# Kernel optimization log

Measured on AMD Instinct MI355X. Metric: run time of the kernel, lower is better.

## Reference

```python
import jax, jax.numpy as jnp
import numpy as np

E = 64      # embedding_dim
H = 64      # h_dim
MLP = 1024  # mlp_dim (attention hidden)
PRE1 = 512  # mlp_pre_pool hidden
BNK = 1024  # bottleneck_dim
S = 256     # num scenes (equal-size groups replacing seq_start_end)
P = 16      # pedestrians per scene
B = S * P   # total batch of pedestrians
T = 8       # obs_len for vx/vy (only last row used)
EPS = 1e-5  # BatchNorm eps


def _bn(x, g, b, m, v):
    # eval-mode BatchNorm1d over the last (feature) axis
    return (x - m) * jax.lax.rsqrt(v + EPS) * g + b


def setup_inputs() -> dict:
    key = jax.random.key(0)
    ks = jax.random.split(key, 24)
    def n(k, shape, s=1.0):
        return jax.random.normal(k, shape, jnp.float32) * s
    return {
        "h_states": n(ks[0], (1, B, H)),
        "end_pos": n(ks[1], (B, 2)),
        "vx": n(ks[2], (T, B)),
        "vy": n(ks[3], (T, B)),
        "W_sp": n(ks[4], (2, E), 0.05), "b_sp": jnp.zeros((E,), jnp.float32),
        "W_vel": n(ks[5], (2, E), 0.05), "b_vel": jnp.zeros((E,), jnp.float32),
        "Wa1": n(ks[6], (2 * E, MLP), 0.05), "ba1": jnp.zeros((MLP,), jnp.float32),
        "ga1": jnp.ones((MLP,), jnp.float32), "bta1": jnp.zeros((MLP,), jnp.float32),
        "ma1": n(ks[7], (MLP,), 0.1), "va1": jax.random.uniform(ks[8], (MLP,), jnp.float32) + 0.5,
        "Wa2": n(ks[9], (MLP, 1), 0.05), "ba2": jnp.zeros((1,), jnp.float32),
        "ga2": jnp.ones((1,), jnp.float32), "bta2": jnp.zeros((1,), jnp.float32),
        "ma2": n(ks[10], (1,), 0.1), "va2": jax.random.uniform(ks[11], (1,), jnp.float32) + 0.5,
        "Wp1": n(ks[12], (E + H, PRE1), 0.05), "bp1": jnp.zeros((PRE1,), jnp.float32),
        "gp1": jnp.ones((PRE1,), jnp.float32), "btp1": jnp.zeros((PRE1,), jnp.float32),
        "mp1": n(ks[13], (PRE1,), 0.1), "vp1": jax.random.uniform(ks[14], (PRE1,), jnp.float32) + 0.5,
        "Wp2": n(ks[15], (PRE1, BNK), 0.05), "bp2": jnp.zeros((BNK,), jnp.float32),
        "gp2": jnp.ones((BNK,), jnp.float32), "btp2": jnp.zeros((BNK,), jnp.float32),
        "mp2": n(ks[16], (BNK,), 0.1), "vp2": jax.random.uniform(ks[17], (BNK,), jnp.float32) + 0.5,
        "num_scenes": S, "num_ped": P,
    }


def _forward(h_states, end_pos, vx, vy, W_sp, b_sp, W_vel, b_vel,
             Wa1, ba1, ga1, bta1, ma1, va1, Wa2, ba2, ga2, bta2, ma2, va2,
             Wp1, bp1, gp1, btp1, mp1, vp1, Wp2, bp2, gp2, btp2, mp2, vp2,
             num_scenes, num_ped):
    Sn, Pn = num_scenes, num_ped
    h = h_states.reshape(-1, H).reshape(Sn, Pn, H)          # per-scene hidden
    pos = end_pos.reshape(Sn, Pn, 2)
    # rel[s,i,j] = pos[s,j] - pos[s,i]  (repeat vs repeat_interleave in torch)
    rel = pos[:, None, :, :] - pos[:, :, None, :]
    rel_emb = rel @ W_sp + b_sp                              # [S,P,P,E]
    vel = jnp.stack([vx[-1], vy[-1]], axis=-1).reshape(Sn, Pn, 2)
    vel_emb = vel @ W_vel + b_vel                            # [S,P,E], indexed by row i
    vel_emb = jnp.broadcast_to(vel_emb[:, :, None, :], (Sn, Pn, Pn, E))
    att_in = jnp.concatenate([rel_emb, vel_emb], axis=-1)    # [S,P,P,2E]
    a = jax.nn.relu(_bn(att_in @ Wa1 + ba1, ga1, bta1, ma1, va1))
    scores = jax.nn.relu(_bn(a @ Wa2 + ba2, ga2, bta2, ma2, va2))  # [S,P,P,1]
    # torch.softmax(scores, dim=1) on an (N,1) tensor: softmax over the size-1
    # feature axis -> identically 1.0. Reproduced faithfully here.
    w = jax.nn.softmax(scores, axis=-1)
    h_rep = jnp.broadcast_to(h[:, None, :, :], (Sn, Pn, Pn, H))   # h[s,j] per (i,j)
    x = jnp.concatenate([rel_emb, h_rep], axis=-1) * (0.05 * w)   # [S,P,P,E+H]
    y = jax.nn.relu(_bn(x @ Wp1 + bp1, gp1, btp1, mp1, vp1))
    y = jax.nn.relu(_bn(y @ Wp2 + bp2, gp2, btp2, mp2, vp2))      # [S,P,P,BNK]
    pool = jnp.max(y, axis=2)                                     # max over neighbors j
    return pool.reshape(Sn * Pn, BNK)


def reference(h_states, end_pos, vx, vy, W_sp, b_sp, W_vel, b_vel,
              Wa1, ba1, ga1, bta1, ma1, va1, Wa2, ba2, ga2, bta2, ma2, va2,
              Wp1, bp1, gp1, btp1, mp1, vp1, Wp2, bp2, gp2, btp2, mp2, vp2,
              num_scenes, num_ped):
    return _forward(h_states, end_pos, vx, vy, W_sp, b_sp, W_vel, b_vel,
                    Wa1, ba1, ga1, bta1, ma1, va1, Wa2, ba2, ga2, bta2, ma2, va2,
                    Wp1, bp1, gp1, btp1, mp1, vp1, Wp2, bp2, gp2, btp2, mp2, vp2,
                    num_scenes, num_ped)
```

## Files before the change

### kernel.cpp

```cpp
#include <hip/hip_runtime.h>
#include <hip/hip_bf16.h>
#include <stdint.h>


typedef __bf16 bf16x8 __attribute__((ext_vector_type(8)));
typedef __bf16 bf16x2 __attribute__((ext_vector_type(2)));
typedef float  f32x4  __attribute__((ext_vector_type(4)));
typedef float  f32x2  __attribute__((ext_vector_type(2)));

#define BP2_OFF 0u
#define BP1_OFF 1048576u
#define MX_OFF  1114112u
#define MY_OFF  1116160u
#define CB_OFF  1118208u
#define SH_OFF  1120256u
#define A2_OFF  1122304u
#define C2_OFF  1126400u

#define Y1_LDS  0
#define HH_LDS  131072
#define LDS_SZ  147456

__device__ __forceinline__ unsigned short f2bf(float f) {
    union { float f; unsigned u; } c; c.f = f;
    unsigned u = c.u;
    return (unsigned short)((u + 0x7fffu + ((u >> 16) & 1u)) >> 16);
}
__device__ __forceinline__ float bfbits2f(unsigned hi) {
    union { unsigned u; float f; } c; c.u = hi; return c.f;
}
__device__ __forceinline__ unsigned pk_bf16(float a, float b) {
#if __has_builtin(__builtin_amdgcn_cvt_pk_bf16_f32)
    bf16x2 p = __builtin_amdgcn_cvt_pk_bf16_f32(a, b);
    union { bf16x2 v; unsigned u; } c; c.v = p; return c.u;
#else
    return (unsigned)f2bf(a) | ((unsigned)f2bf(b) << 16);
#endif
}
__device__ __forceinline__ int y1off(int r, int c16) {
    return r * 1024 + ((c16 ^ (r & 7)) << 4);
}

__global__ __launch_bounds__(256) void prep_pack_kernel(
    const float* __restrict__ Wsp,  const float* __restrict__ bsp,
    const float* __restrict__ Wp1,  const float* __restrict__ bp1,
    const float* __restrict__ gp1,  const float* __restrict__ btp1,
    const float* __restrict__ mp1,  const float* __restrict__ vp1,
    const float* __restrict__ Wp2,  const float* __restrict__ bp2,
    const float* __restrict__ gp2,  const float* __restrict__ btp2,
    const float* __restrict__ mp2,  const float* __restrict__ vp2,
    unsigned char* __restrict__ ws)
{
    __shared__ float tile[32 * 65];
    const int blk = blockIdx.x, t = threadIdx.x;

    if (blk < 272) {
        const float* src; int ncols, kb, ng;
        if (blk < 256) { kb = blk >> 4; ng = blk & 15; src = Wp2; ncols = 1024; }
        else { int b2 = blk - 256; kb = b2 >> 3; ng = b2 & 7; src = Wp1 + 64 * 512; ncols = 512; }
        const int k0 = kb * 32, n0 = ng * 64;
        #pragma unroll
        for (int it = 0; it < 2; ++it) {
            int c = t + it * 256;
            int r = c >> 4, c4 = c & 15;
            float4 v = *(const float4*)(src + (k0 + r) * ncols + n0 + c4 * 4);
            tile[r * 65 + c4 * 4 + 0] = v.x;
            tile[r * 65 + c4 * 4 + 1] = v.y;
            tile[r * 65 + c4 * 4 + 2] = v.z;
            tile[r * 65 + c4 * 4 + 3] = v.w;
        }
        __syncthreads();
        int ntl = t >> 6, l = t & 63;
        int nl = ntl * 16 + (l & 15), kl = (l >> 4) * 8;
        uint4 o;
        o.x = pk_bf16(tile[(kl + 0) * 65 + nl], tile[(kl + 1) * 65 + nl]);
        o.y = pk_bf16(tile[(kl + 2) * 65 + nl], tile[(kl + 3) * 65 + nl]);
        o.z = pk_bf16(tile[(kl + 4) * 65 + nl], tile[(kl + 5) * 65 + nl]);
        o.w = pk_bf16(tile[(kl + 6) * 65 + nl], tile[(kl + 7) * 65 + nl]);
        if (blk < 256) {
            ((uint4*)(ws + BP2_OFF))[(kb * 64 + ng * 4 + ntl) * 64 + l] = o;
        } else {
            ((uint4*)(ws + BP1_OFF))[((ng * 4 + ntl) * 2 + kb) * 64 + l] = o;
        }
    } else if (blk < 274) {
        int k = (blk - 272) * 256 + t;
        float a1 = gp1[k] * rsqrtf(vp1[k] + 1e-5f);
        float mx = 0.f, my = 0.f, cb = 0.f;
        for (int e = 0; e < 64; ++e) {
            float wv = Wp1[e * 512 + k];
            mx = fmaf(Wsp[e],      wv, mx);
            my = fmaf(Wsp[64 + e], wv, my);
            cb = fmaf(bsp[e],      wv, cb);
        }
        ((float*)(ws + MX_OFF))[k] = 0.05f * a1 * mx;
        ((float*)(ws + MY_OFF))[k] = 0.05f * a1 * my;
        ((float*)(ws + CB_OFF))[k] = 0.05f * a1 * cb + (bp1[k] - mp1[k]) * a1 + btp1[k];
        ((float*)(ws + SH_OFF))[k] = 0.05f * a1;
    } else {
        int n = (blk - 274) * 256 + t;
        float a = gp2[n] * rsqrtf(vp2[n] + 1e-5f);
        ((float*)(ws + A2_OFF))[n] = a;
        ((float*)(ws + C2_OFF))[n] = btp2[n] + (bp2[n] - mp2[n]) * a;
    }
}

__global__ __launch_bounds__(512, 2) void mm2_kernel(
    const float* __restrict__ hst,
    const float* __restrict__ epos,
    const unsigned char* __restrict__ ws,
    float* __restrict__ out)
{
    __shared__ __align__(16) unsigned char smem[LDS_SZ];

    const int s   = blockIdx.x >> 1;
    const int ih  = blockIdx.x & 1;
    const int tid = threadIdx.x;
    const int w    = tid >> 6;
    const int l    = tid & 63;
    const int quad = l >> 4;
    const int jl   = l & 15;

    {
        union { unsigned u[4]; bf16x8 v; } afh[2];
        #pragma unroll
        for (int kb = 0; kb < 2; ++kb) {
            const float4* hp = (const float4*)(hst + (s * 16 + jl) * 64 + kb * 32 + quad * 8);
            float4 v0 = hp[0], v1 = hp[1];
            afh[kb].u[0] = pk_bf16(v0.x, v0.y);
            afh[kb].u[1] = pk_bf16(v0.z, v0.w);
            afh[kb].u[2] = pk_bf16(v1.x, v1.y);
            afh[kb].u[3] = pk_bf16(v1.z, v1.w);
        }
        const f32x4 fz = {0.f, 0.f, 0.f, 0.f};
        f32x4 acch[4] = {fz, fz, fz, fz};
        #pragma unroll
        for (int kb = 0; kb < 2; ++kb) {
            #pragma unroll
            for (int ct = 0; ct < 4; ++ct) {
                bf16x8 bfr = *(const bf16x8*)(ws + BP1_OFF + ((((w * 4 + ct) * 2 + kb) * 64 + l) << 4));
                acch[ct] = __builtin_amdgcn_mfma_f32_16x16x32_bf16(afh[kb].v, bfr, acch[ct], 0, 0, 0);
            }
        }
        const float* SHg = (const float*)(ws + SH_OFF);
        const float* CBg = (const float*)(ws + CB_OFF);
        #pragma unroll
        for (int ct = 0; ct < 4; ++ct) {
            int col = (w * 4 + ct) * 16 + jl;
            float sh = SHg[col], cb = CBg[col];
            #pragma unroll
            for (int reg = 0; reg < 4; ++reg) {
                int j = quad * 4 + reg;
                float hv = fmaf(acch[ct][reg], sh, cb);
                *(unsigned short*)(smem + HH_LDS + j * 1024 + col * 2) = f2bf(hv);
            }
        }
    }
    __syncthreads();

    {
        const int i2 = tid >> 8;
        const int j  = (tid >> 4) & 15;
        const int kc = tid & 15;
        float rx[4], ry[4];
        float pjx = epos[s * 32 + j * 2], pjy = epos[s * 32 + j * 2 + 1];
        #pragma unroll
        for (int ii = 0; ii < 4; ++ii) {
            int ig_ = ih * 8 + i2 * 4 + ii;
            rx[ii] = pjx - epos[s * 32 + ig_ * 2];
            ry[ii] = pjy - epos[s * 32 + ig_ * 2 + 1];
        }
        const f32x2 zero2 = {0.f, 0.f};
        #pragma unroll
        for (int kk = 0; kk < 4; ++kk) {
            int k = kc * 32 + kk * 8;
            uint4 hh8 = *(const uint4*)(smem + HH_LDS + j * 1024 + k * 2);
            f32x4 mx0 = *(const f32x4*)(ws + MX_OFF + k * 4);
            f32x4 mx1 = *(const f32x4*)(ws + MX_OFF + k * 4 + 16);
            f32x4 my0 = *(const f32x4*)(ws + MY_OFF + k * 4);
            f32x4 my1 = *(const f32x4*)(ws + MY_OFF + k * 4 + 16);
            f32x2 mxp[4] = { {mx0[0],mx0[1]}, {mx0[2],mx0[3]}, {mx1[0],mx1[1]}, {mx1[2],mx1[3]} };
            f32x2 myp[4] = { {my0[0],my0[1]}, {my0[2],my0[3]}, {my1[0],my1[1]}, {my1[2],my1[3]} };
            f32x2 hhp[4];
            hhp[0][0] = bfbits2f(hh8.x << 16); hhp[0][1] = bfbits2f(hh8.x & 0xffff0000u);
            hhp[1][0] = bfbits2f(hh8.y << 16); hhp[1][1] = bfbits2f(hh8.y & 0xffff0000u);
            hhp[2][0] = bfbits2f(hh8.z << 16); hhp[2][1] = bfbits2f(hh8.z & 0xffff0000u);
            hhp[3][0] = bfbits2f(hh8.w << 16); hhp[3][1] = bfbits2f(hh8.w & 0xffff0000u);
            #pragma unroll
            for (int ii = 0; ii < 4; ++ii) {
                f32x2 rx2 = { rx[ii], rx[ii] };
                f32x2 ry2 = { ry[ii], ry[ii] };
                uint4 o;
                unsigned uu[4];
                #pragma unroll
                for (int p = 0; p < 4; ++p) {
                    f32x2 tt = __builtin_elementwise_fma(ry2, myp[p], hhp[p]);
                    tt = __builtin_elementwise_fma(rx2, mxp[p], tt);
                    tt = __builtin_elementwise_max(tt, zero2);
                    uu[p] = pk_bf16(tt[0], tt[1]);
                }
                o.x = uu[0]; o.y = uu[1]; o.z = uu[2]; o.w = uu[3];
                int r = (i2 * 4 + ii) * 16 + j;
                *(uint4*)(smem + Y1_LDS + y1off(r, kc * 4 + kk)) = o;
            }
        }
    }
    __syncthreads();

    const int ig = w & 1;
    const int ng = w >> 1;
    const float* A2 = (const float*)(ws + A2_OFF);
    const float* C2 = (const float*)(ws + C2_OFF);
    const f32x4 fzero = {0.f, 0.f, 0.f, 0.f};

    int ab[4];
    #pragma unroll
    for (int rt = 0; rt < 4; ++rt) {
        int r = (ig * 4 + rt) * 16 + jl;
        ab[rt] = Y1_LDS + r * 1024 + ((quad ^ (r & 7)) << 4);
    }

    #pragma unroll 1
    for (int chunk = 0; chunk < 2; ++chunk) {
        const int ntbase = ng * 16 + chunk * 8;
        const unsigned char* bp0 = ws + BP2_OFF + (ntbase << 10) + (l << 4);

        f32x4 acc[4][8];
        #pragma unroll
        for (int rt = 0; rt < 4; ++rt)
            #pragma unroll
            for (int ct = 0; ct < 8; ++ct) acc[rt][ct] = fzero;

        bf16x8 b0[8], b1[8];
        #pragma unroll
        for (int ct = 0; ct < 8; ++ct)
            b0[ct] = *(const bf16x8*)(bp0 + ct * 1024);

        #pragma unroll 1
        for (int t = 0; t < 8; ++t) {
            bf16x8 ae[4], ao[4];
            #pragma unroll
            for (int rt = 0; rt < 4; ++rt)
                ae[rt] = *(const bf16x8*)(smem + (ab[rt] + t * 128));
            #pragma unroll
            for (int ct = 0; ct < 8; ++ct)
                b1[ct] = *(const bf16x8*)(bp0 + (2 * t + 1) * 65536 + ct * 1024);
            #pragma unroll
            for (int rt = 0; rt < 4; ++rt)
                ao[rt] = *(const bf16x8*)(smem + ((ab[rt] + t * 128) ^ 64));
            #pragma unroll
            for (int rt = 0; rt < 4; ++rt)
                #pragma unroll
                for (int ct = 0; ct < 8; ++ct)
                    acc[rt][ct] = __builtin_amdgcn_mfma_f32_16x16x32_bf16(ae[rt], b0[ct], acc[rt][ct], 0, 0, 0);
            #pragma unroll
            for (int ct = 0; ct < 8; ++ct)
                b0[ct] = *(const bf16x8*)(bp0 + (2 * t + 2) * 65536 + ct * 1024);
            #pragma unroll
            for (int rt = 0; rt < 4; ++rt)
                #pragma unroll
                for (int ct = 0; ct < 8; ++ct)
                    acc[rt][ct] = __builtin_amdgcn_mfma_f32_16x16x32_bf16(ao[rt], b1[ct], acc[rt][ct], 0, 0, 0);
        }

        #pragma unroll
        for (int ct = 0; ct < 8; ++ct) {
            int col = (ntbase + ct) * 16 + jl;
            float a2 = A2[col], c2 = C2[col];
            #pragma unroll
            for (int rt = 0; rt < 4; ++rt) {
                float v0 = fmaxf(fmaf(acc[rt][ct][0], a2, c2), 0.f);
                float v1 = fmaxf(fmaf(acc[rt][ct][1], a2, c2), 0.f);
                float v2 = fmaxf(fmaf(acc[rt][ct][2], a2, c2), 0.f);
                float v3 = fmaxf(fmaf(acc[rt][ct][3], a2, c2), 0.f);
                float v = fmaxf(fmaxf(v0, v1), fmaxf(v2, v3));
                v = fmaxf(v, __shfl_xor(v, 16, 64));
                v = fmaxf(v, __shfl_xor(v, 32, 64));
                if (l < 16) {
                    int orow = s * 16 + ih * 8 + ig * 4 + rt;
                    __builtin_nontemporal_store(v, &out[orow * 1024 + col]);
                }
            }
        }
    }
}

extern "C" void kernel_launch(void* const* d_in, const int* in_sizes, int n_in,
                              void* d_out, int out_size, void* d_ws, size_t ws_size,
                              hipStream_t stream) {
    const float* hst  = (const float*)d_in[0];
    const float* epos = (const float*)d_in[1];
    const float* Wsp  = (const float*)d_in[4];
    const float* bsp  = (const float*)d_in[5];
    const float* Wp1  = (const float*)d_in[20];
    const float* bp1  = (const float*)d_in[21];
    const float* gp1  = (const float*)d_in[22];
    const float* btp1 = (const float*)d_in[23];
    const float* mp1  = (const float*)d_in[24];
    const float* vp1  = (const float*)d_in[25];
    const float* Wp2  = (const float*)d_in[26];
    const float* bp2  = (const float*)d_in[27];
    const float* gp2  = (const float*)d_in[28];
    const float* btp2 = (const float*)d_in[29];
    const float* mp2  = (const float*)d_in[30];
    const float* vp2  = (const float*)d_in[31];
    unsigned char* ws = (unsigned char*)d_ws;
    float* out = (float*)d_out;

    prep_pack_kernel<<<278, 256, 0, stream>>>(Wsp, bsp, Wp1, bp1, gp1, btp1, mp1, vp1,
                                              Wp2, bp2, gp2, btp2, mp2, vp2, ws);
    mm2_kernel<<<512, 512, 0, stream>>>(hst, epos, ws, out);
}
```

Measured before the change: 199.6 us.

## Switch second MLP GEMM to 32x32x16 MFMA with repacked weights and pipelined loads

Repacks the Wp2 bf16 weight layout for 32-column tiles and rewrites the second-layer GEMM to use 32x32x16 MFMA instead of 16x16x32. Each wave now covers all 128 rows and 4 column tiles. A-operand LDS reads are double-buffered and B-fragment global loads are prefetched three steps ahead, with s_setprio raised around the MFMA bursts. The epilogue max-pool is adapted to the 32x32 accumulator layout. The goal is fewer instructions per FLOP, more operand reuse and better latency hiding. In exchange it holds a larger accumulator footprint and fully unrolls 32 k-steps, which raises register pressure.

After: 246.6 us. 1.24x slower.

```diff
diff --git a/kernel.cpp b/kernel.cpp
--- a/kernel.cpp
+++ b/kernel.cpp
@@ -7,6 +7,7 @@
 typedef __bf16 bf16x2 __attribute__((ext_vector_type(2)));
 typedef float  f32x4  __attribute__((ext_vector_type(4)));
 typedef float  f32x2  __attribute__((ext_vector_type(2)));
+typedef float  f32x16 __attribute__((ext_vector_type(16)));
 
 #define BP2_OFF 0u
 #define BP1_OFF 1048576u
@@ -70,16 +71,25 @@
             tile[r * 65 + c4 * 4 + 3] = v.w;
         }
         __syncthreads();
-        int ntl = t >> 6, l = t & 63;
-        int nl = ntl * 16 + (l & 15), kl = (l >> 4) * 8;
-        uint4 o;
-        o.x = pk_bf16(tile[(kl + 0) * 65 + nl], tile[(kl + 1) * 65 + nl]);
-        o.y = pk_bf16(tile[(kl + 2) * 65 + nl], tile[(kl + 3) * 65 + nl]);
-        o.z = pk_bf16(tile[(kl + 4) * 65 + nl], tile[(kl + 5) * 65 + nl]);
-        o.w = pk_bf16(tile[(kl + 6) * 65 + nl], tile[(kl + 7) * 65 + nl]);
         if (blk < 256) {
-            ((uint4*)(ws + BP2_OFF))[(kb * 64 + ng * 4 + ntl) * 64 + l] = o;
+            const int l = t & 63, ch = (t >> 6) & 1, kh = t >> 7;
+            const int nl = ch * 32 + (l & 31);
+            const int kl = kh * 16 + ((l >> 5) & 1) * 8;
+            uint4 o;
+            o.x = pk_bf16(tile[(kl + 0) * 65 + nl], tile[(kl + 1) * 65 + nl]);
+            o.y = pk_bf16(tile[(kl + 2) * 65 + nl], tile[(kl + 3) * 65 + nl]);
+            o.z = pk_bf16(tile[(kl + 4) * 65 + nl], tile[(kl + 5) * 65 + nl]);
+            o.w = pk_bf16(tile[(kl + 6) * 65 + nl], tile[(kl + 7) * 65 + nl]);
+            const int kstep = kb * 2 + kh, ct = ng * 2 + ch;
+            ((uint4*)(ws + BP2_OFF))[(kstep * 32 + ct) * 64 + l] = o;
         } else {
+            int ntl = t >> 6, l = t & 63;
+            int nl = ntl * 16 + (l & 15), kl = (l >> 4) * 8;
+            uint4 o;
+            o.x = pk_bf16(tile[(kl + 0) * 65 + nl], tile[(kl + 1) * 65 + nl]);
+            o.y = pk_bf16(tile[(kl + 2) * 65 + nl], tile[(kl + 3) * 65 + nl]);
+            o.z = pk_bf16(tile[(kl + 4) * 65 + nl], tile[(kl + 5) * 65 + nl]);
+            o.w = pk_bf16(tile[(kl + 6) * 65 + nl], tile[(kl + 7) * 65 + nl]);
             ((uint4*)(ws + BP1_OFF))[((ng * 4 + ntl) * 2 + kb) * 64 + l] = o;
         }
     } else if (blk < 274) {
@@ -206,78 +216,106 @@
     }
     __syncthreads();
 
-    const int ig = w & 1;
-    const int ng = w >> 1;
-    const float* A2 = (const float*)(ws + A2_OFF);
-    const float* C2 = (const float*)(ws + C2_OFF);
-    const f32x4 fzero = {0.f, 0.f, 0.f, 0.f};
-
-    int ab[4];
-    #pragma unroll
-    for (int rt = 0; rt < 4; ++rt) {
-        int r = (ig * 4 + rt) * 16 + jl;
-        ab[rt] = Y1_LDS + r * 1024 + ((quad ^ (r & 7)) << 4);
-    }
-
-    #pragma unroll 1
-    for (int chunk = 0; chunk < 2; ++chunk) {
-        const int ntbase = ng * 16 + chunk * 8;
-        const unsigned char* bp0 = ws + BP2_OFF + (ntbase << 10) + (l << 4);
-
-        f32x4 acc[4][8];
+    {
+        const int lane31 = l & 31;
+        const int hi = l >> 5;
+        const int sr = lane31 & 7;
+        const float* A2 = (const float*)(ws + A2_OFF);
+        const float* C2 = (const float*)(ws + C2_OFF);
+
+        int av[4][4];
         #pragma unroll
         for (int rt = 0; rt < 4; ++rt)
             #pragma unroll
-            for (int ct = 0; ct < 8; ++ct) acc[rt][ct] = fzero;
-
-        bf16x8 b0[8], b1[8];
-        #pragma unroll
-        for (int ct = 0; ct < 8; ++ct)
-            b0[ct] = *(const bf16x8*)(bp0 + ct * 1024);
+            for (int km = 0; km < 4; ++km)
+                av[rt][km] = Y1_LDS + (rt * 32 + lane31) * 1024
+                           + (((((km << 1) | hi) ^ sr)) << 4);
+
+        const f32x16 fz16 = {0.f,0.f,0.f,0.f,0.f,0.f,0.f,0.f,
+                             0.f,0.f,0.f,0.f,0.f,0.f,0.f,0.f};
 
         #pragma unroll 1
-        for (int t = 0; t < 8; ++t) {
-            bf16x8 ae[4], ao[4];
+        for (int chunk = 0; chunk < 2; ++chunk) {
+            const int ctbase = w * 4 + chunk * 2;
+            const unsigned char* bp = ws + BP2_OFF + (ctbase << 10) + (l << 4);
+
+            f32x16 acc[4][2];
+            #pragma unroll
+            for (int rt = 0; rt < 4; ++rt) { acc[rt][0] = fz16; acc[rt][1] = fz16; }
+
+            bf16x8 aA[4], aB[4];
+            bf16x8 br[3][2];
             #pragma unroll
             for (int rt = 0; rt < 4; ++rt)
-                ae[rt] = *(const bf16x8*)(smem + (ab[rt] + t * 128));
-            #pragma unroll
-            for (int ct = 0; ct < 8; ++ct)
-                b1[ct] = *(const bf16x8*)(bp0 + (2 * t + 1) * 65536 + ct * 1024);
-            #pragma unroll
-            for (int rt = 0; rt < 4; ++rt)
-                ao[rt] = *(const bf16x8*)(smem + ((ab[rt] + t * 128) ^ 64));
-            #pragma unroll
-            for (int rt = 0; rt < 4; ++rt)
+                aA[rt] = *(const bf16x8*)(smem + av[rt][0]);
+            #pragma unroll
+            for (int kp = 0; kp < 3; ++kp) {
+                br[kp][0] = *(const bf16x8*)(bp + kp * 32768);
+                br[kp][1] = *(const bf16x8*)(bp + kp * 32768 + 1024);
+            }
+
+            #pragma unroll
+            for (int k = 0; k < 32; ++k) {
+                if (k < 31) {
+                    const int kn = k + 1;
+                    if ((k & 1) == 0) {
+                        #pragma unroll
+                        for (int rt = 0; rt < 4; ++rt)
+                            aB[rt] = *(const bf16x8*)(smem + av[rt][kn & 3] + (kn >> 2) * 128);
+                    } else {
+                        #pragma unroll
+                        for (int rt = 0; rt < 4; ++rt)
+                            aA[rt] = *(const bf16x8*)(smem + av[rt][kn & 3] + (kn >> 2) * 128);
+                    }
+                }
+                __builtin_amdgcn_s_setprio(1);
+                if ((k & 1) == 0) {
+                    #pragma unroll
+                    for (int c = 0; c < 2; ++c)
+                        #pragma unroll
+                        for (int rt = 0; rt < 4; ++rt)
+                            acc[rt][c] = __builtin_amdgcn_mfma_f32_32x32x16_bf16(
+                                aA[rt], br[k % 3][c], acc[rt][c], 0, 0, 0);
+                } else {
+                    #pragma unroll
+                    for (int c = 0; c < 2; ++c)
+                        #pragma unroll
+                        for (int rt = 0; rt < 4; ++rt)
+                            acc[rt][c] = __builtin_amdgcn_mfma_f32_32x32x16_bf16(
+                                aB[rt], br[k % 3][c], acc[rt][c], 0, 0, 0);
+                }
+                __builtin_amdgcn_s_setprio(0);
+                if (k < 29) {
+                    br[k % 3][0] = *(const bf16x8*)(bp + (k + 3) * 32768);
+                    br[k % 3][1] = *(const bf16x8*)(bp + (k + 3) * 32768 + 1024);
+                }
+            }
+
+            #pragma unroll
+            for (int c = 0; c < 2; ++c) {
+                const int col = (ctbase + c) * 32 + lane31;
+                const float a2 = A2[col], c2v = C2[col];
                 #pragma unroll
-                for (int ct = 0; ct < 8; ++ct)
-                    acc[rt][ct] = __builtin_amdgcn_mfma_f32_16x16x32_bf16(ae[rt], b0[ct], acc[rt][ct], 0, 0, 0);
-            #pragma unroll
-            for (int ct = 0; ct < 8; ++ct)
-                b0[ct] = *(const bf16x8*)(bp0 + (2 * t + 2) * 65536 + ct * 1024);
-            #pragma unroll
-            for (int rt = 0; rt < 4; ++rt)
-                #pragma unroll
-                for (int ct = 0; ct < 8; ++ct)
-                    acc[rt][ct] = __builtin_amdgcn_mfma_f32_16x16x32_bf16(ao[rt], b1[ct], acc[rt][ct], 0, 0, 0);
-        }
-
-        #pragma unroll
-        for (int ct = 0; ct < 8; ++ct) {
-            int col = (ntbase + ct) * 16 + jl;
-            float a2 = A2[col], c2 = C2[col];
-            #pragma unroll
-            for (int rt = 0; rt < 4; ++rt) {
-                float v0 = fmaxf(fmaf(acc[rt][ct][0], a2, c2), 0.f);
-                float v1 = fmaxf(fmaf(acc[rt][ct][1], a2, c2), 0.f);
-                float v2 = fmaxf(fmaf(acc[rt][ct][2], a2, c2), 0.f);
-                float v3 = fmaxf(fmaf(acc[rt][ct][3], a2, c2), 0.f);
-                float v = fmaxf(fmaxf(v0, v1), fmaxf(v2, v3));
-                v = fmaxf(v, __shfl_xor(v, 16, 64));
-                v = fmaxf(v, __shfl_xor(v, 32, 64));
-                if (l < 16) {
-                    int orow = s * 16 + ih * 8 + ig * 4 + rt;
-                    __builtin_nontemporal_store(v, &out[orow * 1024 + col]);
+                for (int rt = 0; rt < 4; ++rt) {
+                    float mv[2];
+                    #pragma unroll
+                    for (int hg = 0; hg < 2; ++hg) {
+                        float v0 = fmaxf(fmaf(acc[rt][c][hg * 8 + 0], a2, c2v), 0.f);
+                        float v1 = fmaxf(fmaf(acc[rt][c][hg * 8 + 1], a2, c2v), 0.f);
+                        float v2 = fmaxf(fmaf(acc[rt][c][hg * 8 + 2], a2, c2v), 0.f);
+                        float v3 = fmaxf(fmaf(acc[rt][c][hg * 8 + 3], a2, c2v), 0.f);
+                        float v4 = fmaxf(fmaf(acc[rt][c][hg * 8 + 4], a2, c2v), 0.f);
+                        float v5 = fmaxf(fmaf(acc[rt][c][hg * 8 + 5], a2, c2v), 0.f);
+                        float v6 = fmaxf(fmaf(acc[rt][c][hg * 8 + 6], a2, c2v), 0.f);
+                        float v7 = fmaxf(fmaf(acc[rt][c][hg * 8 + 7], a2, c2v), 0.f);
+                        float m = fmaxf(fmaxf(fmaxf(v0, v1), fmaxf(v2, v3)),
+                                        fmaxf(fmaxf(v4, v5), fmaxf(v6, v7)));
+                        mv[hg] = fmaxf(m, __shfl_xor(m, 32, 64));
+                    }
+                    const int iloc = rt * 2 + hi;
+                    const float vout = hi ? mv[1] : mv[0];
+                    const int orow = s * 16 + ih * 8 + iloc;
+                    __builtin_nontemporal_store(vout, &out[orow * 1024 + col]);
                 }
             }
         }
```
